# Performance work log

Hardware: AMD Instinct MI355X
Metric: run time of the kernel (lower is better)

## Reference

```python
import jax, jax.numpy as jnp
import numpy as np

_SQRT_2_OVER_PI = 0.7978845608028654  # sqrt(2/pi)
_GELU_COEF = 0.044715
_CLAMP = 3.0  # |x| beyond which GELU is ~identity / ~zero


def setup_inputs() -> dict:
    key = jax.random.key(0)
    x = jax.random.normal(key, (4, 4096, 4096), dtype=jnp.float32)
    return {"input": x}


def _piecewise_gelu(x):
    # middle branch: tanh-approximation GELU
    inner = _SQRT_2_OVER_PI * (x + _GELU_COEF * x * x * x)
    mid = 0.5 * x * (1.0 + jnp.tanh(inner))
    # piecewise: x <= -3 -> 0 ; x >= 3 -> x ; else tanh-GELU
    out = jnp.where(x <= -_CLAMP, jnp.zeros_like(x), mid)
    out = jnp.where(x >= _CLAMP, x, out)
    return out


def reference(input) -> jnp.ndarray:
    return _piecewise_gelu(input)
```

## Files before the change

kernel.cpp:

```cpp
#include <hip/hip_runtime.h>
#include <hip/hip_bf16.h>


typedef float f32x4 __attribute__((ext_vector_type(4)));

#define CLAMP_V 3.0f
#define PG_C0 -2.3022078893f
#define PG_C1 -0.1029432176f

__device__ __forceinline__ float pgelu(float x) {
    float xc = fminf(fmaxf(x, -CLAMP_V), CLAMP_V);
    float x2 = xc * xc;
    float e = __builtin_amdgcn_exp2f(xc * __builtin_fmaf(PG_C1, x2, PG_C0));
    float mid = xc * __builtin_amdgcn_rcpf(1.0f + e);
    float out = (x <= -CLAMP_V) ? 0.0f : mid;
    out = (x >= CLAMP_V) ? x : out;
    return out;
}

__device__ __forceinline__ f32x4 pgelu4(f32x4 v) {
    f32x4 r;
    r.x = pgelu(v.x);
    r.y = pgelu(v.y);
    r.z = pgelu(v.z);
    r.w = pgelu(v.w);
    return r;
}

template <bool NT_LOAD>
__device__ __forceinline__ f32x4 load_chunk(const f32x4* p) {
    if constexpr (NT_LOAD) return __builtin_nontemporal_load(p);
    else return *p;
}

template <bool NT_LOAD>
__global__ __launch_bounds__(256) void pgelu_range(const f32x4* __restrict__ in,
                                                   f32x4* __restrict__ out,
                                                   int start, int end) {
    int stride = gridDim.x * blockDim.x;
    int i = start + blockIdx.x * blockDim.x + threadIdx.x;
    for (; i + 3 * stride < end; i += 4 * stride) {
        f32x4 a0 = load_chunk<NT_LOAD>(&in[i]);
        f32x4 a1 = load_chunk<NT_LOAD>(&in[i + stride]);
        f32x4 a2 = load_chunk<NT_LOAD>(&in[i + 2 * stride]);
        f32x4 a3 = load_chunk<NT_LOAD>(&in[i + 3 * stride]);
        __builtin_nontemporal_store(pgelu4(a0), &out[i]);
        __builtin_nontemporal_store(pgelu4(a1), &out[i + stride]);
        __builtin_nontemporal_store(pgelu4(a2), &out[i + 2 * stride]);
        __builtin_nontemporal_store(pgelu4(a3), &out[i + 3 * stride]);
    }
    for (; i < end; i += stride) {
        f32x4 a = load_chunk<NT_LOAD>(&in[i]);
        __builtin_nontemporal_store(pgelu4(a), &out[i]);
    }
}

__global__ void pgelu_tail(const float* __restrict__ in,
                           float* __restrict__ out, int start, int n) {
    int i = start + blockIdx.x * blockDim.x + threadIdx.x;
    if (i < n) out[i] = pgelu(in[i]);
}

extern "C" void kernel_launch(void* const* d_in, const int* in_sizes, int n_in,
                              void* d_out, int out_size, void* d_ws, size_t ws_size,
                              hipStream_t stream) {
    const float* in = (const float*)d_in[0];
    float* out = (float*)d_out;
    int n = in_sizes[0];
    int n4 = n / 4;

    const int block = 256;
    const int PLAIN_CHUNKS = 12 * 1024 * 1024;

    int plainEnd = n4 < PLAIN_CHUNKS ? n4 : PLAIN_CHUNKS;

    if (plainEnd > 0) {
        int g = (plainEnd + block - 1) / block;
        if (g > 2048) g = 2048;
        pgelu_range<false><<<g, block, 0, stream>>>((const f32x4*)in, (f32x4*)out,
                                                    0, plainEnd);
    }
    if (n4 > plainEnd) {
        int cnt = n4 - plainEnd;
        int g = (cnt + block - 1) / block;
        if (g > 2048) g = 2048;
        pgelu_range<true><<<g, block, 0, stream>>>((const f32x4*)in, (f32x4*)out,
                                                   plainEnd, n4);
    }

    int rem = n - n4 * 4;
    if (rem > 0) {
        pgelu_tail<<<1, 64, 0, stream>>>(in, out, n4 * 4, n);
    }
}
```

Baseline: 98.91 us.

## Merge plain and nontemporal-load launches into one block-contiguous kernel

Replaces the two grid-stride launches (plain loads, then nontemporal loads) with a single kernel. Each block processes one contiguous chunk, and blocks past a three-quarter split point use nontemporal loads. This removes one kernel launch and the gap between launches, and gives each block sequential access to its chunk. In exchange, per-block chunks are large (8192 float4 for this size), so load balance depends on block scheduling, and the cache split point moves from a fixed count to a fraction of the input.

```diff
diff --git a/kernel.cpp b/kernel.cpp
--- a/kernel.cpp
+++ b/kernel.cpp
@@ -34,24 +34,38 @@
 }
 
 template <bool NT_LOAD>
-__global__ __launch_bounds__(256) void pgelu_range(const f32x4* __restrict__ in,
-                                                   f32x4* __restrict__ out,
-                                                   int start, int end) {
-    int stride = gridDim.x * blockDim.x;
-    int i = start + blockIdx.x * blockDim.x + threadIdx.x;
-    for (; i + 3 * stride < end; i += 4 * stride) {
+__device__ __forceinline__ void process_range(const f32x4* __restrict__ in,
+                                              f32x4* __restrict__ out,
+                                              int start, int end) {
+    int i = start + threadIdx.x;
+    for (; i + 768 < end; i += 1024) {
         f32x4 a0 = load_chunk<NT_LOAD>(&in[i]);
-        f32x4 a1 = load_chunk<NT_LOAD>(&in[i + stride]);
-        f32x4 a2 = load_chunk<NT_LOAD>(&in[i + 2 * stride]);
-        f32x4 a3 = load_chunk<NT_LOAD>(&in[i + 3 * stride]);
+        f32x4 a1 = load_chunk<NT_LOAD>(&in[i + 256]);
+        f32x4 a2 = load_chunk<NT_LOAD>(&in[i + 512]);
+        f32x4 a3 = load_chunk<NT_LOAD>(&in[i + 768]);
         __builtin_nontemporal_store(pgelu4(a0), &out[i]);
-        __builtin_nontemporal_store(pgelu4(a1), &out[i + stride]);
-        __builtin_nontemporal_store(pgelu4(a2), &out[i + 2 * stride]);
-        __builtin_nontemporal_store(pgelu4(a3), &out[i + 3 * stride]);
+        __builtin_nontemporal_store(pgelu4(a1), &out[i + 256]);
+        __builtin_nontemporal_store(pgelu4(a2), &out[i + 512]);
+        __builtin_nontemporal_store(pgelu4(a3), &out[i + 768]);
     }
-    for (; i < end; i += stride) {
+    for (; i < end; i += 256) {
         f32x4 a = load_chunk<NT_LOAD>(&in[i]);
         __builtin_nontemporal_store(pgelu4(a), &out[i]);
+    }
+}
+
+__global__ __launch_bounds__(256) void pgelu_blocked(const f32x4* __restrict__ in,
+                                                     f32x4* __restrict__ out,
+                                                     int cpb, int n4,
+                                                     int ntStart) {
+    int start = blockIdx.x * cpb;
+    int end = start + cpb;
+    if (end > n4) end = n4;
+    if (start >= end) return;
+    if (start >= ntStart) {
+        process_range<true>(in, out, start, end);
+    } else {
+        process_range<false>(in, out, start, end);
     }
 }
 
@@ -69,23 +83,14 @@
     int n = in_sizes[0];
     int n4 = n / 4;
 
-    const int block = 256;
-    const int PLAIN_CHUNKS = 12 * 1024 * 1024;
-
-    int plainEnd = n4 < PLAIN_CHUNKS ? n4 : PLAIN_CHUNKS;
-
-    if (plainEnd > 0) {
-        int g = (plainEnd + block - 1) / block;
-        if (g > 2048) g = 2048;
-        pgelu_range<false><<<g, block, 0, stream>>>((const f32x4*)in, (f32x4*)out,
-                                                    0, plainEnd);
-    }
-    if (n4 > plainEnd) {
-        int cnt = n4 - plainEnd;
-        int g = (cnt + block - 1) / block;
-        if (g > 2048) g = 2048;
-        pgelu_range<true><<<g, block, 0, stream>>>((const f32x4*)in, (f32x4*)out,
-                                                   plainEnd, n4);
+    if (n4 > 0) {
+        long long cpbL = ((long long)n4 + 2047) / 2048;
+        cpbL = (cpbL + 1023) & ~1023LL;
+        int cpb = (int)cpbL;
+        int grid = (int)((n4 + cpb - 1) / cpb);
+        int ntStart = (int)(((long long)n4 * 3 / 4) / cpb * cpb);
+        pgelu_blocked<<<grid, 256, 0, stream>>>((const f32x4*)in, (f32x4*)out,
+                                                cpb, n4, ntStart);
     }
 
     int rem = n - n4 * 4;
```

Measured after the change: 89.23 us. -9.8%, faster.
